# Kernel tuning notes

Hardware: AMD Instinct MI355X
Metric: run time of the kernel (lower is better)

## Reference

```python
import jax, jax.numpy as jnp
import numpy as np

HIDDEN = 1024
HEADS = 16
HEAD_DIM = HIDDEN // HEADS
EPS = 1e-5


def setup_inputs() -> dict:
    key = jax.random.key(0)
    ks = jax.random.split(key, 9)
    B, S, H = 2, 2048, HIDDEN
    scale = 1.0 / np.sqrt(H)
    inp = {
        "hidden_states": jax.random.normal(ks[0], (B, S, H), dtype=jnp.float32),
        "Wq": jax.random.normal(ks[1], (H, H), dtype=jnp.float32) * scale,
        "bq": jnp.zeros((H,), jnp.float32),
        "Wk": jax.random.normal(ks[2], (H, H), dtype=jnp.float32) * scale,
        "bk": jnp.zeros((H,), jnp.float32),
        "Wv": jax.random.normal(ks[3], (H, H), dtype=jnp.float32) * scale,
        "bv": jnp.zeros((H,), jnp.float32),
        "Wo": jax.random.normal(ks[4], (H, H), dtype=jnp.float32) * scale,
        "bo": jnp.zeros((H,), jnp.float32),
        "gamma": jnp.ones((H,), jnp.float32),
        "beta": jnp.zeros((H,), jnp.float32),
    }
    return inp


def reference(hidden_states, Wq, bq, Wk, bk, Wv, bv, Wo, bo, gamma, beta):
    B, S, H = hidden_states.shape
    residual = hidden_states

    def shape(x):  # [B,S,H] -> [B,heads,S,head_dim]
        return x.reshape(B, S, HEADS, HEAD_DIM).transpose(0, 2, 1, 3)

    q = shape(hidden_states @ Wq + bq)
    k = shape(hidden_states @ Wk + bk)
    v = shape(hidden_states @ Wv + bv)

    scores = jnp.einsum("bhqd,bhkd->bhqk", q, k) / jnp.sqrt(
        jnp.asarray(HEAD_DIM, hidden_states.dtype))
    probs = jax.nn.softmax(scores, axis=-1)
    context = jnp.einsum("bhqk,bhkd->bhqd", probs, v)
    context = context.transpose(0, 2, 1, 3).reshape(B, S, H)

    output = context @ Wo + bo
    x = output + residual
    mu = jnp.mean(x, axis=-1, keepdims=True)
    var = jnp.mean(jnp.square(x - mu), axis=-1, keepdims=True)
    return (x - mu) * jax.lax.rsqrt(var + EPS) * gamma + beta
```

## Files before the change

kernel.cpp:

```cpp
#include <hip/hip_runtime.h>
#include <hip/hip_bf16.h>
#include <math.h>

#define HIDDEN 1024
#define HEADS 16
#define HEAD_DIM 64
#define EPS 1e-5f

typedef __attribute__((ext_vector_type(8))) short bf16x8;
typedef __attribute__((ext_vector_type(4))) float f32x4;

#if defined(__has_builtin)
#if __has_builtin(__builtin_amdgcn_exp2f)
#define EXP2(x) __builtin_amdgcn_exp2f(x)
#endif
#endif
#ifndef EXP2
#define EXP2(x) exp2f(x)
#endif

#define QSCALE 0.18033688011112042f

__device__ __forceinline__ short f2bf(float f) {
    union { float f; unsigned u; } v; v.f = f;
    unsigned r = v.u + 0x7fffu + ((v.u >> 16) & 1u);
    return (short)(r >> 16);
}

__device__ __forceinline__ void gl_lds16(const void* g, void* l) {
    __builtin_amdgcn_global_load_lds(
        (const __attribute__((address_space(1))) void*)g,
        (__attribute__((address_space(3))) void*)l, 16, 0, 0);
}

__global__ __launch_bounds__(256) void prep_kernel(
    const float* __restrict__ X,
    const float* __restrict__ Wq, const float* __restrict__ Wk,
    const float* __restrict__ Wv, const float* __restrict__ Wo,
    const float* __restrict__ bq, const float* __restrict__ bk,
    const float* __restrict__ bv,
    short* __restrict__ Xb, short* __restrict__ Wt3, short* __restrict__ Wot,
    float* __restrict__ b3)
{
    const int z = blockIdx.z;
    __shared__ short tile[32][33];
    if (z < 4) {
        const float* W = (z == 0) ? Wq : (z == 1) ? Wk : (z == 2) ? Wv : Wo;
        short* dst = (z < 3) ? (Wt3 + (size_t)z * 1024 * 1024) : Wot;
        const float scale = (z == 0) ? QSCALE : 1.0f;
        int n0 = blockIdx.x * 32, k0 = blockIdx.y * 32;
        int tx = threadIdx.x & 31, ty = threadIdx.x >> 5;
        #pragma unroll
        for (int i = 0; i < 32; i += 8)
            tile[ty + i][tx] = f2bf(W[(size_t)(k0 + ty + i) * 1024 + n0 + tx] * scale);
        __syncthreads();
        #pragma unroll
        for (int i = 0; i < 32; i += 8)
            dst[(size_t)(n0 + ty + i) * 1024 + k0 + tx] = tile[tx][ty + i];
    } else if (z < 8) {
        int l = (z - 4) * 1024 + blockIdx.y * 32 + blockIdx.x;
        int i = (l * 256 + threadIdx.x) * 4;
        float4 v = *(const float4*)(X + i);
        short o[4] = { f2bf(v.x), f2bf(v.y), f2bf(v.z), f2bf(v.w) };
        *(uint2*)(Xb + i) = *(uint2*)o;
    } else {
        int i = (blockIdx.y * 32 + blockIdx.x) * 256 + threadIdx.x;
        if (i < 3072) {
            float v = (i < 1024) ? bq[i] * QSCALE
                    : (i < 2048) ? bk[i - 1024] : bv[i - 2048];
            b3[i] = v;
        }
    }
}

template<int BM>
__global__ __launch_bounds__(256) void gemm_bt_mfma(
    const short* __restrict__ A, const short* __restrict__ Bt,
    const float* __restrict__ bias,
    void* __restrict__ C0, int ldc0,
    void* __restrict__ C1, int split_col, int ldc1, int c1_trans,
    const float* __restrict__ resid,
    int M, int N, int K, int out_bf16)
{
    constexpr int MT = BM / 32;
    constexpr int ACH = BM / 32;
    __shared__ short As[2][BM * 64];
    __shared__ short Bs[2][128 * 64];
    const int tid = threadIdx.x;
    const int wave = tid >> 6, lane = tid & 63;
    const int ln16 = lane & 15, quad = lane >> 4;
    const int wm = (wave >> 1) * (BM / 2), wn = (wave & 1) * 64;

    const int gx = gridDim.x;
    int bid = blockIdx.y * gx + blockIdx.x;
    const int cpx = (gx * gridDim.y) >> 3;
    bid = (bid & 7) * cpx + (bid >> 3);
    const int brow = (bid / gx) * BM, bcol = (bid % gx) * 128;

    const int kr  = lane >> 3;
    const int kb8 = lane & 7;

    f32x4 acc[MT][4];
    #pragma unroll
    for (int mt = 0; mt < MT; ++mt)
        #pragma unroll
        for (int nt = 0; nt < 4; ++nt) acc[mt][nt] = (f32x4){0.f, 0.f, 0.f, 0.f};

    auto stage = [&](int p, int kt) {
        #pragma unroll
        for (int i = 0; i < ACH; ++i) {
            int ci = wave * ACH + i;
            int r  = ci * 8 + kr;
            int csrc = (kb8 ^ (r & 7)) * 8;
            gl_lds16(A + (size_t)(brow + r) * K + kt * 64 + csrc, &As[p][ci * 512]);
        }
        #pragma unroll
        for (int i = 0; i < 4; ++i) {
            int ci = wave * 4 + i;
            int r  = ci * 8 + kr;
            int csrc = (kb8 ^ (r & 7)) * 8;
            gl_lds16(Bt + (size_t)(bcol + r) * K + kt * 64 + csrc, &Bs[p][ci * 512]);
        }
    };

    const int NKT = K / 64;
    stage(0, 0);

    for (int kt = 0; kt < NKT; ++kt) {
        const int cur = kt & 1;
        asm volatile("s_waitcnt vmcnt(0)" ::: "memory");
        __builtin_amdgcn_s_barrier();
        __builtin_amdgcn_sched_barrier(0);
        if (kt + 1 < NKT) stage(cur ^ 1, kt + 1);

        #pragma unroll
        for (int kk = 0; kk < 2; ++kk) {
            bf16x8 af[MT], bf[4];
            #pragma unroll
            for (int mt = 0; mt < MT; ++mt) {
                int r = wm + mt * 16 + ln16;
                af[mt] = *(const bf16x8*)&As[cur][r * 64 + (((kk * 4 + quad) ^ (r & 7)) * 8)];
            }
            #pragma unroll
            for (int nt = 0; nt < 4; ++nt) {
                int r = wn + nt * 16 + ln16;
                bf[nt] = *(const bf16x8*)&Bs[cur][r * 64 + (((kk * 4 + quad) ^ (r & 7)) * 8)];
            }
            #pragma unroll
            for (int mt = 0; mt < MT; ++mt)
                #pragma unroll
                for (int nt = 0; nt < 4; ++nt)
                    acc[mt][nt] = __builtin_amdgcn_mfma_f32_16x16x32_bf16(
                        af[mt], bf[nt], acc[mt][nt], 0, 0, 0);
        }
    }

    if (bcol >= split_col && c1_trans) {
        #pragma unroll
        for (int mt = 0; mt < MT; ++mt) {
            int row0 = brow + wm + mt * 16 + quad * 4;
            #pragma unroll
            for (int nt = 0; nt < 4; ++nt) {
                int col = bcol + wn + nt * 16 + ln16;
                float bv = bias[col];
                short o4[4];
                #pragma unroll
                for (int r = 0; r < 4; ++r) o4[r] = f2bf(acc[mt][nt][r] + bv);
                *(uint2*)((short*)C1 + (size_t)(col - split_col) * ldc1 + row0) =
                    *(uint2*)o4;
            }
        }
        return;
    }

    void* Cp = C0; int ld = ldc0; int coff = 0;
    if (bcol >= split_col) { Cp = C1; ld = ldc1; coff = split_col; }

    #pragma unroll
    for (int mt = 0; mt < MT; ++mt) {
        #pragma unroll
        for (int r = 0; r < 4; ++r) {
            int row = brow + wm + mt * 16 + quad * 4 + r;
            #pragma unroll
            for (int nt = 0; nt < 4; ++nt) {
                int col = bcol + wn + nt * 16 + ln16;
                float v = acc[mt][nt][r] + bias[col];
                if (resid) v += resid[(size_t)row * N + col];
                if (out_bf16) ((short*)Cp)[(size_t)row * ld + (col - coff)] = f2bf(v);
                else          ((float*)Cp)[(size_t)row * ld + (col - coff)] = v;
            }
        }
    }
}

__global__ __launch_bounds__(256, 2) void attn_mfma_kernel(
    const short* __restrict__ QKb, const short* __restrict__ VT,
    short* __restrict__ Ctx)
{
    const int S = 2048;
    const int h = blockIdx.x, qt = blockIdx.y, b = blockIdx.z;
    const int tid = threadIdx.x;
    const int wave = tid >> 6, lane = tid & 63;
    const int ln16 = lane & 15, quad = lane >> 4;

    __shared__ alignas(16) char smem[81920];
    char* Pw = smem + 65536 + wave * 4096;

    bf16x8 qf[4][2];
    #pragma unroll
    for (int qg = 0; qg < 4; ++qg)
        #pragma unroll
        for (int kb = 0; kb < 2; ++kb)
            qf[qg][kb] = *(const bf16x8*)(QKb +
                (size_t)(b * S + qt * 64 + qg * 16 + ln16) * 2048 +
                h * 64 + kb * 32 + quad * 8);

    f32x4 of[4][4];
    float rs[4] = {0.f, 0.f, 0.f, 0.f};
    #pragma unroll
    for (int qg = 0; qg < 4; ++qg)
        #pragma unroll
        for (int nt = 0; nt < 4; ++nt) of[qg][nt] = (f32x4){0.f, 0.f, 0.f, 0.f};

    auto stage = [&](int p, int kt) {
        short* ksb = (short*)(smem + p * 16384);
        short* vsb = (short*)(smem + 32768 + p * 16384);
        const int kr  = lane >> 3;
        const int kb8 = lane & 7;
        const int vr  = lane >> 4;
        const int vb16 = lane & 15;
        #pragma unroll
        for (int i = 0; i < 4; ++i) {
            int r = wave * 32 + i * 8 + kr;
            int ksrc = (kb8 ^ (r & 7)) * 8;
            gl_lds16(QKb + (size_t)(b * S + kt * 128 + r) * 2048 + 1024 + h * 64 + ksrc,
                     ksb + (wave * 32 + i * 8) * 64);
            int d = wave * 16 + i * 4 + vr;
            int vsrc = (vb16 ^ (d & 15)) * 8;
            gl_lds16(VT + (size_t)(h * 64 + d) * 4096 + b * S + kt * 128 + vsrc,
                     vsb + (wave * 16 + i * 4) * 128);
        }
    };

    stage(0, 0);

    const int t0w = wave * 32;

    for (int kt = 0; kt < 16; ++kt) {
        const int cur = kt & 1;
        asm volatile("s_waitcnt vmcnt(0)" ::: "memory");
        __builtin_amdgcn_s_barrier();
        __builtin_amdgcn_sched_barrier(0);
        if (kt + 1 < 16) stage(cur ^ 1, kt + 1);

        const short* ks = (const short*)(smem + cur * 16384);
        const short* vs = (const short*)(smem + 32768 + cur * 16384);

        #pragma unroll
        for (int kblk = 0; kblk < 2; ++kblk) {
            int rloc = t0w + kblk * 16 + ln16;
            bf16x8 kf0 = *(const bf16x8*)&ks[rloc * 64 + ((quad ^ (rloc & 7)) * 8)];
            bf16x8 kf1 = *(const bf16x8*)&ks[rloc * 64 + (((4 + quad) ^ (rloc & 7)) * 8)];
            #pragma unroll
            for (int qg = 0; qg < 4; ++qg) {
                f32x4 a = (f32x4){0.f, 0.f, 0.f, 0.f};
                __builtin_amdgcn_s_setprio(1);
                a = __builtin_amdgcn_mfma_f32_16x16x32_bf16(kf0, qf[qg][0], a, 0, 0, 0);
                a = __builtin_amdgcn_mfma_f32_16x16x32_bf16(kf1, qf[qg][1], a, 0, 0, 0);
                __builtin_amdgcn_s_setprio(0);
                float p0 = EXP2(a[0]), p1 = EXP2(a[1]);
                float p2 = EXP2(a[2]), p3 = EXP2(a[3]);
                rs[qg] += (p0 + p1) + (p2 + p3);
                union { __hip_bfloat162 h2; unsigned u; } c01, c23;
                c01.h2 = __float22bfloat162_rn(make_float2(p0, p1));
                c23.h2 = __float22bfloat162_rn(make_float2(p2, p3));
                uint2 w; w.x = c01.u; w.y = c23.u;
                int qrow = qg * 16 + ln16;
                int key = (qrow >> 1) & 3;
                int bblk = (kblk * 2 + (quad >> 1)) ^ key;
                *(uint2*)(Pw + qrow * 64 + bblk * 16 + (quad & 1) * 8) = w;
            }
        }

        bf16x8 pf[4];
        #pragma unroll
        for (int qg = 0; qg < 4; ++qg) {
            int qrow = qg * 16 + ln16;
            int key = (qrow >> 1) & 3;
            pf[qg] = *(const bf16x8*)(Pw + qrow * 64 + ((quad ^ key) * 16));
        }
        __builtin_amdgcn_s_setprio(1);
        #pragma unroll
        for (int nt = 0; nt < 4; ++nt) {
            int d = nt * 16 + ln16;
            bf16x8 vf = *(const bf16x8*)&vs[d * 128 + (((wave * 4 + quad) ^ (d & 15)) * 8)];
            #pragma unroll
            for (int qg = 0; qg < 4; ++qg)
                of[qg][nt] = __builtin_amdgcn_mfma_f32_16x16x32_bf16(pf[qg], vf, of[qg][nt], 0, 0, 0);
        }
        __builtin_amdgcn_s_setprio(0);
    }

    __syncthreads();

    #pragma unroll
    for (int qg = 0; qg < 4; ++qg) {
        rs[qg] += __shfl_xor(rs[qg], 16, 64);
        rs[qg] += __shfl_xor(rs[qg], 32, 64);
    }

    float* Rw = (float*)(smem + wave * 4864);
    float* Lb = (float*)(smem + 4 * 4864);

    if (quad == 0) {
        #pragma unroll
        for (int qg = 0; qg < 4; ++qg)
            Lb[wave * 64 + qg * 16 + ln16] = rs[qg];
    }

    const int rq  = tid >> 2;
    const int rd0 = (tid & 3) * 4;
    float inv = 0.f;

    #pragma unroll
    for (int nt = 0; nt < 4; ++nt) {
        #pragma unroll
        for (int qg = 0; qg < 4; ++qg)
            #pragma unroll
            for (int r = 0; r < 4; ++r)
                Rw[(qg * 16 + quad * 4 + r) * 19 + ln16] = of[qg][nt][r];
        __syncthreads();
        if (nt == 0) {
            float l = Lb[rq] + Lb[64 + rq] + Lb[128 + rq] + Lb[192 + rq];
            inv = 1.f / l;
        }
        short o4[4];
        #pragma unroll
        for (int j = 0; j < 4; ++j) {
            int d = rd0 + j;
            float s = 0.f;
            #pragma unroll
            for (int w = 0; w < 4; ++w)
                s += ((const float*)(smem + w * 4864))[rq * 19 + d];
            o4[j] = f2bf(s * inv);
        }
        *(uint2*)(Ctx + (size_t)(b * S + qt * 64 + rq) * 1024 + h * 64 + nt * 16 + rd0) =
            *(uint2*)o4;
        __syncthreads();
    }
}

__global__ __launch_bounds__(256) void resln_kernel(
    const float* __restrict__ xin, const float* __restrict__ gamma,
    const float* __restrict__ beta, float* __restrict__ out)
{
    const int row = blockIdx.x;
    const int tid = threadIdx.x;
    const int wid = tid >> 6, lane = tid & 63;
    __shared__ float red[8];

    float4 x = *(const float4*)(xin + (size_t)row * HIDDEN + tid * 4);
    float s = x.x + x.y + x.z + x.w;
    #pragma unroll
    for (int off = 32; off > 0; off >>= 1) s += __shfl_xor(s, off, 64);
    if (lane == 0) red[wid] = s;
    __syncthreads();
    float mu = (red[0] + red[1] + red[2] + red[3]) * (1.f / HIDDEN);

    float dx = x.x - mu, dy = x.y - mu, dz = x.z - mu, dw = x.w - mu;
    float v = dx * dx + dy * dy + dz * dz + dw * dw;
    #pragma unroll
    for (int off = 32; off > 0; off >>= 1) v += __shfl_xor(v, off, 64);
    if (lane == 0) red[4 + wid] = v;
    __syncthreads();
    float var = (red[4] + red[5] + red[6] + red[7]) * (1.f / HIDDEN);
    float rstd = rsqrtf(var + EPS);

    float4 g = *(const float4*)(gamma + tid * 4);
    float4 bt = *(const float4*)(beta + tid * 4);
    float4 o;
    o.x = dx * rstd * g.x + bt.x;
    o.y = dy * rstd * g.y + bt.y;
    o.z = dz * rstd * g.z + bt.z;
    o.w = dw * rstd * g.w + bt.w;
    *(float4*)(out + (size_t)row * HIDDEN + tid * 4) = o;
}

extern "C" void kernel_launch(void* const* d_in, const int* in_sizes, int n_in,
                              void* d_out, int out_size, void* d_ws, size_t ws_size,
                              hipStream_t stream)
{
    const float* X     = (const float*)d_in[0];
    const float* Wq    = (const float*)d_in[1];
    const float* bq    = (const float*)d_in[2];
    const float* Wk    = (const float*)d_in[3];
    const float* bk    = (const float*)d_in[4];
    const float* Wv    = (const float*)d_in[5];
    const float* bv    = (const float*)d_in[6];
    const float* Wo    = (const float*)d_in[7];
    const float* bo    = (const float*)d_in[8];
    const float* gamma = (const float*)d_in[9];
    const float* beta  = (const float*)d_in[10];
    float* out = (float*)d_out;

    const int B = 2, S = 2048;
    const int M = B * S;

    char* ws = (char*)d_ws;
    short* Xb  = (short*)(ws);
    short* Ctx = (short*)(ws);
    short* Wot = (short*)(ws + (8ull << 20));
    short* Wt3 = (short*)(ws + (10ull << 20));
    float* b3  = (float*)(ws + (16ull << 20));
    short* QKb = (short*)(ws + (17ull << 20));
    float* Pj  = (float*)(ws + (17ull << 20));
    short* VT  = (short*)(ws + (33ull << 20));

    dim3 blk(256);

    prep_kernel<<<dim3(32, 32, 9), blk, 0, stream>>>(
        X, Wq, Wk, Wv, Wo, bq, bk, bv, Xb, Wt3, Wot, b3);

    dim3 qkvgrid(3072 / 128, M / 128);
    gemm_bt_mfma<128><<<qkvgrid, blk, 0, stream>>>(Xb, Wt3, b3,
                                              QKb, 2048, VT, 2048, 4096, 1,
                                              nullptr, M, 3072, HIDDEN, 1);

    dim3 agrid(HEADS, S / 64, B);
    attn_mfma_kernel<<<agrid, blk, 0, stream>>>(QKb, VT, Ctx);

    dim3 ogrid(HIDDEN / 128, M / 64);
    gemm_bt_mfma<64><<<ogrid, blk, 0, stream>>>(Ctx, Wot, bo,
                                            Pj, 1024, nullptr, 1 << 30, 0, 0,
                                            X, M, HIDDEN, HIDDEN, 0);

    resln_kernel<<<M, blk, 0, stream>>>(Pj, gamma, beta, out);
}
```

Measured before the change: 227.1 us.

## Restructure attention to per-wave query rows with single-buffered 64-key tiles

```diff
diff --git a/kernel.cpp b/kernel.cpp
--- a/kernel.cpp
+++ b/kernel.cpp
@@ -193,7 +193,7 @@
     }
 }
 
-__global__ __launch_bounds__(256, 2) void attn_mfma_kernel(
+__global__ __launch_bounds__(256) void attn_mfma_kernel(
     const short* __restrict__ QKb, const short* __restrict__ VT,
     short* __restrict__ Ctx)
 {
@@ -203,150 +203,114 @@
     const int wave = tid >> 6, lane = tid & 63;
     const int ln16 = lane & 15, quad = lane >> 4;
 
-    __shared__ alignas(16) char smem[81920];
-    char* Pw = smem + 65536 + wave * 4096;
-
-    bf16x8 qf[4][2];
-    #pragma unroll
-    for (int qg = 0; qg < 4; ++qg)
+    __shared__ short Ks[64 * 64];
+    __shared__ short Vs[64 * 64];
+    __shared__ short Ps[128 * 72];
+
+    const int q0 = qt * 128 + wave * 32;
+
+    bf16x8 qfrag[2][2];
+    #pragma unroll
+    for (int qg = 0; qg < 2; ++qg)
         #pragma unroll
         for (int kb = 0; kb < 2; ++kb)
-            qf[qg][kb] = *(const bf16x8*)(QKb +
-                (size_t)(b * S + qt * 64 + qg * 16 + ln16) * 2048 +
-                h * 64 + kb * 32 + quad * 8);
-
-    f32x4 of[4][4];
-    float rs[4] = {0.f, 0.f, 0.f, 0.f};
-    #pragma unroll
-    for (int qg = 0; qg < 4; ++qg)
+            qfrag[qg][kb] = *(const bf16x8*)(QKb +
+                (size_t)(b * S + q0 + qg * 16 + ln16) * 2048 + h * 64 + kb * 32 + quad * 8);
+
+    bf16x8 ones;
+    #pragma unroll
+    for (int j = 0; j < 8; ++j) ones[j] = (short)0x3F80;
+
+    f32x4 of[2][4], lacc[2];
+    #pragma unroll
+    for (int qg = 0; qg < 2; ++qg) {
+        lacc[qg] = (f32x4){0.f, 0.f, 0.f, 0.f};
         #pragma unroll
         for (int nt = 0; nt < 4; ++nt) of[qg][nt] = (f32x4){0.f, 0.f, 0.f, 0.f};
-
-    auto stage = [&](int p, int kt) {
-        short* ksb = (short*)(smem + p * 16384);
-        short* vsb = (short*)(smem + 32768 + p * 16384);
-        const int kr  = lane >> 3;
-        const int kb8 = lane & 7;
-        const int vr  = lane >> 4;
-        const int vb16 = lane & 15;
-        #pragma unroll
-        for (int i = 0; i < 4; ++i) {
-            int r = wave * 32 + i * 8 + kr;
-            int ksrc = (kb8 ^ (r & 7)) * 8;
-            gl_lds16(QKb + (size_t)(b * S + kt * 128 + r) * 2048 + 1024 + h * 64 + ksrc,
-                     ksb + (wave * 32 + i * 8) * 64);
-            int d = wave * 16 + i * 4 + vr;
-            int vsrc = (vb16 ^ (d & 15)) * 8;
-            gl_lds16(VT + (size_t)(h * 64 + d) * 4096 + b * S + kt * 128 + vsrc,
-                     vsb + (wave * 16 + i * 4) * 128);
-        }
-    };
-
-    stage(0, 0);
-
-    const int t0w = wave * 32;
-
-    for (int kt = 0; kt < 16; ++kt) {
-        const int cur = kt & 1;
-        asm volatile("s_waitcnt vmcnt(0)" ::: "memory");
-        __builtin_amdgcn_s_barrier();
-        __builtin_amdgcn_sched_barrier(0);
-        if (kt + 1 < 16) stage(cur ^ 1, kt + 1);
-
-        const short* ks = (const short*)(smem + cur * 16384);
-        const short* vs = (const short*)(smem + 32768 + cur * 16384);
-
-        #pragma unroll
-        for (int kblk = 0; kblk < 2; ++kblk) {
-            int rloc = t0w + kblk * 16 + ln16;
-            bf16x8 kf0 = *(const bf16x8*)&ks[rloc * 64 + ((quad ^ (rloc & 7)) * 8)];
-            bf16x8 kf1 = *(const bf16x8*)&ks[rloc * 64 + (((4 + quad) ^ (rloc & 7)) * 8)];
-            #pragma unroll
-            for (int qg = 0; qg < 4; ++qg) {
+    }
+
+    const int sr  = lane >> 3;
+    const int scb = lane & 7;
+
+    for (int kt = 0; kt < S / 64; ++kt) {
+        __syncthreads();
+        #pragma unroll
+        for (int i = 0; i < 2; ++i) {
+            int ci = wave * 2 + i;
+            int r  = ci * 8 + sr;
+            int csrc = ((scb ^ (r & 7))) * 8;
+            gl_lds16(QKb + (size_t)(b * S + kt * 64 + r) * 2048 + 1024 + h * 64 + csrc,
+                     &Ks[ci * 512]);
+            gl_lds16(VT + (size_t)(h * 64 + r) * 4096 + b * S + kt * 64 + csrc,
+                     &Vs[ci * 512]);
+        }
+        __syncthreads();
+
+        #pragma unroll
+        for (int nt = 0; nt < 4; ++nt) {
+            bf16x8 kf[2];
+            #pragma unroll
+            for (int kb = 0; kb < 2; ++kb) {
+                int r = nt * 16 + ln16;
+                int cb = (kb * 4 + quad) ^ (r & 7);
+                kf[kb] = *(const bf16x8*)&Ks[r * 64 + cb * 8];
+            }
+            #pragma unroll
+            for (int qg = 0; qg < 2; ++qg) {
                 f32x4 a = (f32x4){0.f, 0.f, 0.f, 0.f};
-                __builtin_amdgcn_s_setprio(1);
-                a = __builtin_amdgcn_mfma_f32_16x16x32_bf16(kf0, qf[qg][0], a, 0, 0, 0);
-                a = __builtin_amdgcn_mfma_f32_16x16x32_bf16(kf1, qf[qg][1], a, 0, 0, 0);
-                __builtin_amdgcn_s_setprio(0);
+                a = __builtin_amdgcn_mfma_f32_16x16x32_bf16(kf[0], qfrag[qg][0], a, 0, 0, 0);
+                a = __builtin_amdgcn_mfma_f32_16x16x32_bf16(kf[1], qfrag[qg][1], a, 0, 0, 0);
                 float p0 = EXP2(a[0]), p1 = EXP2(a[1]);
                 float p2 = EXP2(a[2]), p3 = EXP2(a[3]);
-                rs[qg] += (p0 + p1) + (p2 + p3);
                 union { __hip_bfloat162 h2; unsigned u; } c01, c23;
                 c01.h2 = __float22bfloat162_rn(make_float2(p0, p1));
                 c23.h2 = __float22bfloat162_rn(make_float2(p2, p3));
                 uint2 w; w.x = c01.u; w.y = c23.u;
-                int qrow = qg * 16 + ln16;
-                int key = (qrow >> 1) & 3;
-                int bblk = (kblk * 2 + (quad >> 1)) ^ key;
-                *(uint2*)(Pw + qrow * 64 + bblk * 16 + (quad & 1) * 8) = w;
-            }
-        }
-
-        bf16x8 pf[4];
-        #pragma unroll
-        for (int qg = 0; qg < 4; ++qg) {
-            int qrow = qg * 16 + ln16;
-            int key = (qrow >> 1) & 3;
-            pf[qg] = *(const bf16x8*)(Pw + qrow * 64 + ((quad ^ key) * 16));
-        }
-        __builtin_amdgcn_s_setprio(1);
+                *(uint2*)&Ps[(wave * 32 + qg * 16 + ln16) * 72 + nt * 16 + quad * 4] = w;
+            }
+        }
+
+        bf16x8 pf[2][2];
+        #pragma unroll
+        for (int qg = 0; qg < 2; ++qg)
+            #pragma unroll
+            for (int kb = 0; kb < 2; ++kb)
+                pf[qg][kb] = *(const bf16x8*)
+                    &Ps[(wave * 32 + qg * 16 + ln16) * 72 + kb * 32 + quad * 8];
+
+        #pragma unroll
+        for (int qg = 0; qg < 2; ++qg) {
+            lacc[qg] = __builtin_amdgcn_mfma_f32_16x16x32_bf16(pf[qg][0], ones, lacc[qg], 0, 0, 0);
+            lacc[qg] = __builtin_amdgcn_mfma_f32_16x16x32_bf16(pf[qg][1], ones, lacc[qg], 0, 0, 0);
+        }
         #pragma unroll
         for (int nt = 0; nt < 4; ++nt) {
-            int d = nt * 16 + ln16;
-            bf16x8 vf = *(const bf16x8*)&vs[d * 128 + (((wave * 4 + quad) ^ (d & 15)) * 8)];
-            #pragma unroll
-            for (int qg = 0; qg < 4; ++qg)
-                of[qg][nt] = __builtin_amdgcn_mfma_f32_16x16x32_bf16(pf[qg], vf, of[qg][nt], 0, 0, 0);
-        }
-        __builtin_amdgcn_s_setprio(0);
-    }
-
-    __syncthreads();
-
-    #pragma unroll
-    for (int qg = 0; qg < 4; ++qg) {
-        rs[qg] += __shfl_xor(rs[qg], 16, 64);
-        rs[qg] += __shfl_xor(rs[qg], 32, 64);
-    }
-
-    float* Rw = (float*)(smem + wave * 4864);
-    float* Lb = (float*)(smem + 4 * 4864);
-
-    if (quad == 0) {
-        #pragma unroll
-        for (int qg = 0; qg < 4; ++qg)
-            Lb[wave * 64 + qg * 16 + ln16] = rs[qg];
-    }
-
-    const int rq  = tid >> 2;
-    const int rd0 = (tid & 3) * 4;
-    float inv = 0.f;
-
-    #pragma unroll
-    for (int nt = 0; nt < 4; ++nt) {
-        #pragma unroll
-        for (int qg = 0; qg < 4; ++qg)
-            #pragma unroll
-            for (int r = 0; r < 4; ++r)
-                Rw[(qg * 16 + quad * 4 + r) * 19 + ln16] = of[qg][nt][r];
-        __syncthreads();
-        if (nt == 0) {
-            float l = Lb[rq] + Lb[64 + rq] + Lb[128 + rq] + Lb[192 + rq];
-            inv = 1.f / l;
-        }
-        short o4[4];
-        #pragma unroll
-        for (int j = 0; j < 4; ++j) {
-            int d = rd0 + j;
-            float s = 0.f;
-            #pragma unroll
-            for (int w = 0; w < 4; ++w)
-                s += ((const float*)(smem + w * 4864))[rq * 19 + d];
-            o4[j] = f2bf(s * inv);
-        }
-        *(uint2*)(Ctx + (size_t)(b * S + qt * 64 + rq) * 1024 + h * 64 + nt * 16 + rd0) =
-            *(uint2*)o4;
-        __syncthreads();
+            bf16x8 vf[2];
+            #pragma unroll
+            for (int kb = 0; kb < 2; ++kb) {
+                int r = nt * 16 + ln16;
+                int cb = (kb * 4 + quad) ^ (r & 7);
+                vf[kb] = *(const bf16x8*)&Vs[r * 64 + cb * 8];
+            }
+            #pragma unroll
+            for (int qg = 0; qg < 2; ++qg) {
+                of[qg][nt] = __builtin_amdgcn_mfma_f32_16x16x32_bf16(pf[qg][0], vf[0], of[qg][nt], 0, 0, 0);
+                of[qg][nt] = __builtin_amdgcn_mfma_f32_16x16x32_bf16(pf[qg][1], vf[1], of[qg][nt], 0, 0, 0);
+            }
+        }
+    }
+
+    #pragma unroll
+    for (int qg = 0; qg < 2; ++qg) {
+        #pragma unroll
+        for (int r = 0; r < 4; ++r) {
+            float inv = 1.f / lacc[qg][r];
+            int row = b * S + qt * 128 + wave * 32 + qg * 16 + quad * 4 + r;
+            #pragma unroll
+            for (int nt = 0; nt < 4; ++nt)
+                Ctx[(size_t)row * 1024 + h * 64 + nt * 16 + ln16] =
+                    f2bf(of[qg][nt][r] * inv);
+        }
     }
 }
 
@@ -421,12 +385,12 @@
     prep_kernel<<<dim3(32, 32, 9), blk, 0, stream>>>(
         X, Wq, Wk, Wv, Wo, bq, bk, bv, Xb, Wt3, Wot, b3);
 
-    dim3 qkvgrid(3072 / 128, M / 128);
-    gemm_bt_mfma<128><<<qkvgrid, blk, 0, stream>>>(Xb, Wt3, b3,
+    dim3 qkvgrid(3072 / 128, M / 64);
+    gemm_bt_mfma<64><<<qkvgrid, blk, 0, stream>>>(Xb, Wt3, b3,
                                               QKb, 2048, VT, 2048, 4096, 1,
                                               nullptr, M, 3072, HIDDEN, 1);
 
-    dim3 agrid(HEADS, S / 64, B);
+    dim3 agrid(HEADS, S / 128, B);
     attn_mfma_kernel<<<agrid, blk, 0, stream>>>(QKb, VT, Ctx);
 
     dim3 ogrid(HIDDEN / 128, M / 64);
```

After: 220.9 us. 2.7% less time.
